# Kernel tuning notes

Measured on AMD Instinct MI355X. Metric: run time of the kernel, lower is better.

The kernel has to match this reference:

```python
import jax, jax.numpy as jnp
import numpy as np

EPS = 1e-6
SLIDING_WINDOW = 512
ROPE_BASE = 10000.0  # rope_local_base_freq for sliding_attention layers


def _rms_norm(x, w=None):
    # Gemma-style RMSNorm computed in fp32 then cast back
    xf = x.astype(jnp.float32)
    out = xf * jax.lax.rsqrt(jnp.mean(xf * xf, axis=-1, keepdims=True) + EPS)
    if w is not None:
        out = out * w.astype(jnp.float32)
    return out.astype(x.dtype)


def _rotate_half(x):
    x1, x2 = jnp.split(x, 2, axis=-1)
    return jnp.concatenate((-x2, x1), axis=-1)


def setup_inputs() -> dict:
    key = jax.random.key(0)
    ks = jax.random.split(key, 6)
    B, S, H, NH, NKV, D = 1, 4096, 2048, 8, 2, 256
    hidden_states = jax.random.normal(ks[0], (B, S, H), dtype=jnp.float32)
    w_q = jax.random.normal(ks[1], (H, NH * D), dtype=jnp.float32) * 0.02
    w_k = jax.random.normal(ks[2], (H, NKV * D), dtype=jnp.float32) * 0.02
    w_v = jax.random.normal(ks[3], (H, NKV * D), dtype=jnp.float32) * 0.02
    w_o = jax.random.normal(ks[4], (NH * D, H), dtype=jnp.float32) * 0.02
    q_norm_w = jnp.ones((D,), dtype=jnp.float32)
    k_norm_w = jnp.ones((D,), dtype=jnp.float32)
    # RoPE tables (local base freq, sliding layer)
    inv_freq = 1.0 / (ROPE_BASE ** (jnp.arange(0, D, 2, dtype=jnp.float32) / D))
    pos = jnp.arange(S, dtype=jnp.float32)
    freqs = pos[:, None] * inv_freq[None, :]          # [S, D/2]
    emb = jnp.concatenate((freqs, freqs), axis=-1)    # [S, D]
    cos = jnp.broadcast_to(jnp.cos(emb)[None], (B, S, D)).astype(jnp.float32)
    sin = jnp.broadcast_to(jnp.sin(emb)[None], (B, S, D)).astype(jnp.float32)
    return {"hidden_states": hidden_states, "w_q": w_q, "w_k": w_k, "w_v": w_v,
            "w_o": w_o, "q_norm_w": q_norm_w, "k_norm_w": k_norm_w,
            "cos": cos, "sin": sin}


def reference(hidden_states, w_q, w_k, w_v, w_o, q_norm_w, k_norm_w, cos, sin):
    B, S, _ = hidden_states.shape
    D = cos.shape[-1]
    NH = w_q.shape[1] // D
    NKV = w_k.shape[1] // D
    G = NH // NKV

    # projections -> [B, S, heads, D], per-head RMSNorm (Gemma3n-style)
    q = _rms_norm((hidden_states @ w_q).reshape(B, S, NH, D), q_norm_w)
    k = _rms_norm((hidden_states @ w_k).reshape(B, S, NKV, D), k_norm_w)
    v = _rms_norm((hidden_states @ w_v).reshape(B, S, NKV, D))  # v_norm: no scale

    q = q.transpose(0, 2, 1, 3)  # [B, NH, S, D]
    k = k.transpose(0, 2, 1, 3)  # [B, NKV, S, D]
    v = v.transpose(0, 2, 1, 3)

    # RoPE, cos/sin unsqueezed over the head dim
    c = cos[:, None, :, :]
    s = sin[:, None, :, :]
    q = q * c + _rotate_half(q) * s
    k = k * c + _rotate_half(k) * s

    # GQA: repeat KV heads
    k = jnp.repeat(k, G, axis=1)  # [B, NH, S, D]
    v = jnp.repeat(v, G, axis=1)

    # attention, scaling = 1.0 (q_norm replaces 1/sqrt(d) in this family)
    scores = jnp.einsum('bhqd,bhkd->bhqk', q, k)

    # causal + sliding-window mask
    i = jnp.arange(S)[:, None]
    j = jnp.arange(S)[None, :]
    mask = (j <= i) & ((i - j) < SLIDING_WINDOW)
    scores = jnp.where(mask[None, None], scores, jnp.finfo(scores.dtype).min)

    attn = jax.nn.softmax(scores.astype(jnp.float32), axis=-1).astype(q.dtype)
    out = jnp.einsum('bhqk,bhkd->bhqd', attn, v)
    out = out.transpose(0, 2, 1, 3).reshape(B, S, NH * D)
    return out @ w_o
```

## Files before the change

### kernel.cpp

```cpp
#include <hip/hip_runtime.h>
#include <hip/hip_bf16.h>

#define S_LEN 4096
#define HDIM  2048
#define NHQ   8
#define NKVH  2
#define DHEAD 256
#define WIN   512
#define NQKV  3072

typedef __hip_bfloat16 bf16_t;
using fragAB = __attribute__((ext_vector_type(8))) short;
using fragC  = __attribute__((ext_vector_type(4))) float;

typedef unsigned int u32;
typedef const __attribute__((address_space(1))) u32* gas_ptr;
typedef __attribute__((address_space(3))) u32* las_ptr;

__device__ __forceinline__ void async_copy16(const void* g, void* l) {
  __builtin_amdgcn_global_load_lds((gas_ptr)g, (las_ptr)l, 16, 0, 0);
}

#define NEG_BIG (-3.0e38f)

__device__ __forceinline__ void split2(float x, bf16_t& hi, bf16_t& lo) {
  bf16_t h = __float2bfloat16(x);
  hi = h;
  lo = __float2bfloat16(x - (float)h);
}

__global__ __launch_bounds__(256) void split_f32(
    const float* __restrict__ in, bf16_t* __restrict__ hi,
    bf16_t* __restrict__ lo, int n) {
  int i = (blockIdx.x * 256 + threadIdx.x) * 4;
  if (i >= n) return;
  float4 v = *(const float4*)(in + i);
  split2(v.x, hi[i + 0], lo[i + 0]);
  split2(v.y, hi[i + 1], lo[i + 1]);
  split2(v.z, hi[i + 2], lo[i + 2]);
  split2(v.w, hi[i + 3], lo[i + 3]);
}

__global__ __launch_bounds__(256) void transpose_cvt(
    const float* __restrict__ in, bf16_t* __restrict__ out, int R, int C) {
  __shared__ bf16_t tile[32][33];
  int c0 = blockIdx.x * 32, r0 = blockIdx.y * 32;
  int tx = threadIdx.x & 31, ty = threadIdx.x >> 5;
#pragma unroll
  for (int i = 0; i < 4; ++i)
    tile[ty + i * 8][tx] = __float2bfloat16(in[(size_t)(r0 + ty + i * 8) * C + c0 + tx]);
  __syncthreads();
#pragma unroll
  for (int i = 0; i < 4; ++i)
    out[(size_t)(c0 + ty + i * 8) * R + r0 + tx] = tile[tx][ty + i * 8];
}

__global__ __launch_bounds__(256) void transpose_split(
    const float* __restrict__ in, bf16_t* __restrict__ hiT,
    bf16_t* __restrict__ loT, int R, int C) {
  __shared__ bf16_t th[32][33];
  __shared__ bf16_t tl[32][33];
  int c0 = blockIdx.x * 32, r0 = blockIdx.y * 32;
  int tx = threadIdx.x & 31, ty = threadIdx.x >> 5;
#pragma unroll
  for (int i = 0; i < 4; ++i) {
    float x = in[(size_t)(r0 + ty + i * 8) * C + c0 + tx];
    bf16_t h, l; split2(x, h, l);
    th[ty + i * 8][tx] = h;
    tl[ty + i * 8][tx] = l;
  }
  __syncthreads();
#pragma unroll
  for (int i = 0; i < 4; ++i) {
    hiT[(size_t)(c0 + ty + i * 8) * R + r0 + tx] = th[tx][ty + i * 8];
    loT[(size_t)(c0 + ty + i * 8) * R + r0 + tx] = tl[tx][ty + i * 8];
  }
}

#define VMCNT_(n) asm volatile("s_waitcnt vmcnt(" #n ")" ::: "memory")
#define VMCNT(n) VMCNT_(n)
#define BARRIER()                     \
  {                                   \
    asm volatile("" ::: "memory");    \
    __builtin_amdgcn_s_barrier();     \
    asm volatile("" ::: "memory");    \
  }

#define MFMA_(a, b, c) __builtin_amdgcn_mfma_f32_16x16x32_bf16(a, b, c, 0, 0, 0)

#define OFF_AH 0
#define OFF_AL 16384
#define OFF_BH 32768
#define OFF_BL 45056
#define BUFSZ  57344

#define LOADB()                                                   \
  _Pragma("unroll")                                               \
  for (int j = 0; j < 3; ++j) {                                   \
    const char* bp_ = bufc + (wn + j * 16 + l16) * 64 + rdq;      \
    bh[j] = *(const fragAB*)(bp_ + OFF_BH);                       \
    bl[j] = *(const fragAB*)(bp_ + OFF_BL);                       \
  }

struct ARegs { fragAB ah0, al0, ah1, al1; };

__device__ __forceinline__ void lda_split(ARegs& r, const char* bufc, int wm,
                                          int p, int l16, int rdq) {
  const char* a0 = bufc + (wm + (2 * p) * 16 + l16) * 64 + rdq;
  const char* a1 = a0 + 16 * 64;
  r.ah0 = *(const fragAB*)(a0 + OFF_AH);
  r.al0 = *(const fragAB*)(a0 + OFF_AL);
  r.ah1 = *(const fragAB*)(a1 + OFF_AH);
  r.al1 = *(const fragAB*)(a1 + OFF_AL);
}

__device__ __forceinline__ void mfma_split(fragC (&acc)[8][3], const ARegs& r,
                                           const fragAB (&bh)[3],
                                           const fragAB (&bl)[3], int p) {
  __builtin_amdgcn_s_setprio(1);
#pragma unroll
  for (int j = 0; j < 3; ++j) {
    acc[2 * p][j]     = MFMA_(r.al0, bh[j], acc[2 * p][j]);
    acc[2 * p + 1][j] = MFMA_(r.al1, bh[j], acc[2 * p + 1][j]);
  }
#pragma unroll
  for (int j = 0; j < 3; ++j) {
    acc[2 * p][j]     = MFMA_(r.ah0, bl[j], acc[2 * p][j]);
    acc[2 * p + 1][j] = MFMA_(r.ah1, bl[j], acc[2 * p + 1][j]);
  }
#pragma unroll
  for (int j = 0; j < 3; ++j) {
    acc[2 * p][j]     = MFMA_(r.ah0, bh[j], acc[2 * p][j]);
    acc[2 * p + 1][j] = MFMA_(r.ah1, bh[j], acc[2 * p + 1][j]);
  }
  __builtin_amdgcn_s_setprio(0);
}

#define SPLIT_STEP()                        \
  {                                         \
    LOADB();                                \
    lda_split(r0, bufc, wm, 0, l16, rdq);   \
    lda_split(r1, bufc, wm, 1, l16, rdq);   \
    mfma_split(acc, r0, bh, bl, 0);         \
    lda_split(r0, bufc, wm, 2, l16, rdq);   \
    mfma_split(acc, r1, bh, bl, 1);         \
    lda_split(r1, bufc, wm, 3, l16, rdq);   \
    mfma_split(acc, r0, bh, bl, 2);         \
    mfma_split(acc, r1, bh, bl, 3);         \
  }

__global__ __launch_bounds__(512, 2) void gemm_split2(
    const bf16_t* __restrict__ Ah, const bf16_t* __restrict__ Al,
    const bf16_t* __restrict__ Bh, const bf16_t* __restrict__ Bl,
    float* __restrict__ C, int M, int N, int K) {
  __shared__ __align__(16) char lds[2 * BUFSZ];
  const int t = threadIdx.x;
  const int wave = t >> 6, lane = t & 63;
  const int quad = lane >> 4, l16 = lane & 15;
  const int m0 = blockIdx.y * 256, n0 = blockIdx.x * 192;
  const int wm = (wave >> 2) * 128, wn = (wave & 3) * 48;
  const int rdq = (quad ^ ((l16 >> 1) & 3)) * 16;

  const size_t laneOff =
      (size_t)(lane >> 2) * K * 2 + 16 * ((lane & 3) ^ ((lane >> 3) & 3));

  const char* gsrc[7];
  int ldsOff[7];
#pragma unroll
  for (int pos = 0; pos < 3; ++pos) {
    int c = wave + 8 * pos;
    if (c < 12) {
      gsrc[pos]   = (const char*)Bh + (size_t)(n0 + 16 * c) * K * 2 + laneOff;
      ldsOff[pos] = OFF_BH + c * 1024;
    } else {
      gsrc[pos]   = (const char*)Bl + (size_t)(n0 + 16 * (c - 12)) * K * 2 + laneOff;
      ldsOff[pos] = OFF_BL + (c - 12) * 1024;
    }
  }
#pragma unroll
  for (int p = 0; p < 4; ++p) {
    int sub = wave & 3;
    int R0 = ((sub >> 1) & 1) * 128 + 32 * p + (sub & 1) * 16;
    const char* base = (const char*)(wave < 4 ? Ah : Al);
    gsrc[3 + p]   = base + (size_t)(m0 + R0) * K * 2 + laneOff;
    ldsOff[3 + p] = (wave < 4 ? OFF_AH : OFF_AL) + R0 * 64;
  }

  fragC zero4 = {0.f, 0.f, 0.f, 0.f};
  fragC acc[8][3];
#pragma unroll
  for (int i = 0; i < 8; ++i)
#pragma unroll
    for (int j = 0; j < 3; ++j) acc[i][j] = zero4;

  char* ldsc = (char*)lds;
#pragma unroll
  for (int ps = 0; ps < 7; ++ps) async_copy16(gsrc[ps], ldsc + ldsOff[ps]);
#pragma unroll
  for (int ps = 0; ps < 7; ++ps) gsrc[ps] += 64;

  fragAB bh[3], bl[3];
  ARegs r0, r1;
  int cur = 0;
  const int NS = K / 32;
  for (int it = 0; it < NS - 1; ++it) {
    const char* bufc = ldsc + cur * BUFSZ;
    char* nb = ldsc + (cur ^ 1) * BUFSZ;
    VMCNT(0); BARRIER();
#pragma unroll
    for (int ps = 0; ps < 7; ++ps) async_copy16(gsrc[ps], nb + ldsOff[ps]);
#pragma unroll
    for (int ps = 0; ps < 7; ++ps) gsrc[ps] += 64;
    SPLIT_STEP();
    cur ^= 1;
  }
  {
    const char* bufc = ldsc + cur * BUFSZ;
    VMCNT(0); BARRIER();
    SPLIT_STEP();
  }

#pragma unroll
  for (int i = 0; i < 8; ++i)
#pragma unroll
    for (int j = 0; j < 3; ++j)
#pragma unroll
      for (int r = 0; r < 4; ++r) {
        int row = m0 + wm + i * 16 + quad * 4 + r;
        int col = n0 + wn + j * 16 + l16;
        C[(size_t)row * N + col] = acc[i][j][r];
      }
}

#define BT_OFF_A 0
#define BT_OFF_B 32768
#define BT_BUFSZ 49152

struct ARegs2 { fragAB a[2][2]; };

__device__ __forceinline__ void lda_bt(ARegs2& r, const char* bufc, int wm,
                                       int p, int l16, int quad, int rx) {
#pragma unroll
  for (int u = 0; u < 2; ++u)
#pragma unroll
    for (int ks = 0; ks < 2; ++ks)
      r.a[u][ks] = *(const fragAB*)(bufc + BT_OFF_A +
                                    (wm + (2 * p + u) * 16 + l16) * 128 +
                                    (((ks * 4 + quad) ^ rx) * 16));
}

__device__ __forceinline__ void mfma_bt(fragC (&acc)[8][2], const ARegs2& r,
                                        const fragAB (&b)[2][2], int p) {
  __builtin_amdgcn_s_setprio(1);
#pragma unroll
  for (int ks = 0; ks < 2; ++ks)
#pragma unroll
    for (int j = 0; j < 2; ++j) {
      acc[2 * p][j]     = MFMA_(r.a[0][ks], b[j][ks], acc[2 * p][j]);
      acc[2 * p + 1][j] = MFMA_(r.a[1][ks], b[j][ks], acc[2 * p + 1][j]);
    }
  __builtin_amdgcn_s_setprio(0);
}

#define BT_LOADB()                                                        \
  _Pragma("unroll")                                                       \
  for (int j = 0; j < 2; ++j)                                             \
  _Pragma("unroll")                                                       \
    for (int ks = 0; ks < 2; ++ks)                                        \
      bfr[j][ks] = *(const fragAB*)(bufc + BT_OFF_B +                     \
                                    (wn + j * 16 + l16) * 128 +           \
                                    (((ks * 4 + quad) ^ rx) * 16));

#define BT_STEP()                                 \
  {                                               \
    BT_LOADB();                                   \
    lda_bt(r0, bufc, wm, 0, l16, quad, rx);       \
    lda_bt(r1, bufc, wm, 1, l16, quad, rx);       \
    mfma_bt(acc, r0, bfr, 0);                     \
    lda_bt(r0, bufc, wm, 2, l16, quad, rx);       \
    mfma_bt(acc, r1, bfr, 1);                     \
    lda_bt(r1, bufc, wm, 3, l16, quad, rx);       \
    mfma_bt(acc, r0, bfr, 2);                     \
    mfma_bt(acc, r1, bfr, 3);                     \
  }

__global__ __launch_bounds__(512, 2) void gemm_bt2(
    const bf16_t* __restrict__ A, const bf16_t* __restrict__ Bt,
    float* __restrict__ C, int M, int N, int K) {
  __shared__ __align__(16) char lds[2 * BT_BUFSZ];
  const int t = threadIdx.x;
  const int wave = t >> 6, lane = t & 63;
  const int quad = lane >> 4, l16 = lane & 15;
  const int m0 = blockIdx.y * 256, n0 = blockIdx.x * 128;
  const int wm = (wave >> 2) * 128, wn = (wave & 3) * 32;
  const int rx = l16 & 7;

  const size_t laneOff =
      (size_t)(lane >> 3) * K * 2 + 16 * ((lane & 7) ^ ((lane >> 3) & 7));

  const char* gsrc[6];
  int ldsOff[6];
#pragma unroll
  for (int pos = 0; pos < 2; ++pos) {
    int c = wave + 8 * pos;
    gsrc[pos]   = (const char*)Bt + (size_t)(n0 + 8 * c) * K * 2 + laneOff;
    ldsOff[pos] = BT_OFF_B + c * 1024;
  }
#pragma unroll
  for (int p = 0; p < 4; ++p) {
    int R0 = (wave >> 2) * 128 + 32 * p + (wave & 3) * 8;
    gsrc[2 + p]   = (const char*)A + (size_t)(m0 + R0) * K * 2 + laneOff;
    ldsOff[2 + p] = BT_OFF_A + R0 * 128;
  }

  fragC zero4 = {0.f, 0.f, 0.f, 0.f};
  fragC acc[8][2];
#pragma unroll
  for (int i = 0; i < 8; ++i)
#pragma unroll
    for (int j = 0; j < 2; ++j) acc[i][j] = zero4;

  char* ldsc = (char*)lds;
#pragma unroll
  for (int ps = 0; ps < 6; ++ps) async_copy16(gsrc[ps], ldsc + ldsOff[ps]);
#pragma unroll
  for (int ps = 0; ps < 6; ++ps) gsrc[ps] += 128;

  fragAB bfr[2][2];
  ARegs2 r0, r1;
  int cur = 0;
  const int NS = K / 64;
  for (int it = 0; it < NS - 1; ++it) {
    const char* bufc = ldsc + cur * BT_BUFSZ;
    char* nb = ldsc + (cur ^ 1) * BT_BUFSZ;
    VMCNT(0); BARRIER();
#pragma unroll
    for (int ps = 0; ps < 6; ++ps) async_copy16(gsrc[ps], nb + ldsOff[ps]);
#pragma unroll
    for (int ps = 0; ps < 6; ++ps) gsrc[ps] += 128;
    BT_STEP();
    cur ^= 1;
  }
  {
    const char* bufc = ldsc + cur * BT_BUFSZ;
    VMCNT(0); BARRIER();
    BT_STEP();
  }

#pragma unroll
  for (int i = 0; i < 8; ++i)
#pragma unroll
    for (int j = 0; j < 2; ++j)
#pragma unroll
      for (int r = 0; r < 4; ++r) {
        int row = m0 + wm + i * 16 + quad * 4 + r;
        int col = n0 + wn + j * 16 + l16;
        C[(size_t)row * N + col] = acc[i][j][r];
      }
}

__global__ __launch_bounds__(256) void rmsnorm_rope_split(
    const float* __restrict__ proj, const float* __restrict__ w,
    const float* __restrict__ cosb, const float* __restrict__ sinb,
    bf16_t* __restrict__ qhi, bf16_t* __restrict__ qlo,
    int inStride, int inOff, int outStride) {
  int s = blockIdx.x, h = blockIdx.y, d = threadIdx.x;
  float x = proj[(size_t)s * inStride + inOff + h * DHEAD + d];
  float ss = x * x;
  ss += __shfl_xor(ss, 1);  ss += __shfl_xor(ss, 2);  ss += __shfl_xor(ss, 4);
  ss += __shfl_xor(ss, 8);  ss += __shfl_xor(ss, 16); ss += __shfl_xor(ss, 32);
  __shared__ float part[4];
  __shared__ float xs[DHEAD];
  if ((threadIdx.x & 63) == 0) part[threadIdx.x >> 6] = ss;
  __syncthreads();
  float tot = part[0] + part[1] + part[2] + part[3];
  float r = rsqrtf(tot * (1.0f / DHEAD) + 1e-6f);
  float xn = x * r * w[d];
  xs[d] = xn;
  __syncthreads();
  float other = xs[(d + 128) & 255];
  float rot = (d < 128) ? -other : other;
  float y = xn * cosb[(size_t)s * DHEAD + d] + rot * sinb[(size_t)s * DHEAD + d];
  bf16_t h2, l2; split2(y, h2, l2);
  size_t oidx = (size_t)s * outStride + h * DHEAD + d;
  qhi[oidx] = h2;
  qlo[oidx] = l2;
}

__global__ __launch_bounds__(256) void rmsnorm_vT(
    const float* __restrict__ proj, bf16_t* __restrict__ vt,
    int inStride, int inOff) {
  int s = blockIdx.x, h = blockIdx.y, d = threadIdx.x;
  float x = proj[(size_t)s * inStride + inOff + h * DHEAD + d];
  float ss = x * x;
  ss += __shfl_xor(ss, 1);  ss += __shfl_xor(ss, 2);  ss += __shfl_xor(ss, 4);
  ss += __shfl_xor(ss, 8);  ss += __shfl_xor(ss, 16); ss += __shfl_xor(ss, 32);
  __shared__ float part[4];
  if ((threadIdx.x & 63) == 0) part[threadIdx.x >> 6] = ss;
  __syncthreads();
  float tot = part[0] + part[1] + part[2] + part[3];
  float r = rsqrtf(tot * (1.0f / DHEAD) + 1e-6f);
  vt[((size_t)h * DHEAD + d) * S_LEN + s] = __float2bfloat16(x * r);
}

__global__ __launch_bounds__(256) void attn_split(
    const bf16_t* __restrict__ Qhi, const bf16_t* __restrict__ Qlo,
    const bf16_t* __restrict__ Khi, const bf16_t* __restrict__ Klo,
    const bf16_t* __restrict__ Vt, bf16_t* __restrict__ Aout) {
  const int h = blockIdx.y;
  const int qb = blockIdx.x * 64;
  const int wave = threadIdx.x >> 6, lane = threadIdx.x & 63;
  const int quad = lane >> 4, l16 = lane & 15;
  const int qw = qb + wave * 16;
  const int kv = h >> 2;
  const bf16_t* Qh_ = Qhi + h * DHEAD;
  const bf16_t* Ql_ = Qlo + h * DHEAD;
  const bf16_t* Kh_ = Khi + kv * DHEAD;
  const bf16_t* Kl_ = Klo + kv * DHEAD;
  const bf16_t* Vh_ = Vt + (size_t)kv * DHEAD * S_LEN;

  __shared__ __align__(16) bf16_t KshH[32 * 256];
  __shared__ __align__(16) bf16_t KshL[32 * 256];
  __shared__ __align__(16) bf16_t Vsh[256 * 32];
  __shared__ __align__(16) bf16_t Plds[4][16 * 32];

  fragAB qfh[8], qfl[8];
#pragma unroll
  for (int c = 0; c < 8; ++c) {
    size_t off = (size_t)(qw + l16) * (NHQ * DHEAD) + c * 32 + quad * 8;
    qfh[c] = *(const fragAB*)(Qh_ + off);
    qfl[c] = *(const fragAB*)(Ql_ + off);
  }

  int kRow[4], kCol[4], vRow[4], vCol[4];
#pragma unroll
  for (int i = 0; i < 4; ++i) {
    int ci = (i * 4 + wave) * 64 + lane;
    int r = ci >> 5, sc = ci & 31;
    kRow[i] = r;
    kCol[i] = (sc ^ r) * 8;
    int rv = ci >> 2, scv = ci & 3;
    vRow[i] = rv;
    vCol[i] = (scv ^ (rv & 3)) * 8;
  }

  fragC zero4 = {0.f, 0.f, 0.f, 0.f};
  fragC o_acc[16];
#pragma unroll
  for (int c = 0; c < 16; ++c) o_acc[c] = zero4;
  float m_run[4] = {NEG_BIG, NEG_BIG, NEG_BIG, NEG_BIG};
  float l_run[4] = {0.f, 0.f, 0.f, 0.f};
  const float LOG2E = 1.4426950408889634f;

  int k_lo = qb - (WIN - 1);
  if (k_lo < 0) k_lo = 0;
  k_lo &= ~31;

  for (int kb = k_lo; kb < qb + 64; kb += 32) {
#pragma unroll
    for (int i = 0; i < 4; ++i) {
      size_t dst = (size_t)(i * 4 + wave) * 1024;
      size_t koff = (size_t)(kb + kRow[i]) * (NKVH * DHEAD) + kCol[i];
      async_copy16(Kh_ + koff, (char*)KshH + dst);
      async_copy16(Kl_ + koff, (char*)KshL + dst);
      async_copy16(Vh_ + (size_t)vRow[i] * S_LEN + kb + vCol[i], (char*)Vsh + dst);
    }
    __syncthreads();

    fragC s0 = zero4, s1 = zero4;
#pragma unroll
    for (int c = 0; c < 8; ++c) {
      int j = c * 4 + quad;
      int off0 = (l16 * 32 + (j ^ l16)) * 16;
      int off1 = ((16 + l16) * 32 + (j ^ (16 + l16))) * 16;
      fragAB kh0 = *(const fragAB*)((const char*)KshH + off0);
      fragAB kl0 = *(const fragAB*)((const char*)KshL + off0);
      fragAB kh1 = *(const fragAB*)((const char*)KshH + off1);
      fragAB kl1 = *(const fragAB*)((const char*)KshL + off1);
      s0 = __builtin_amdgcn_mfma_f32_16x16x32_bf16(qfl[c], kh0, s0, 0, 0, 0);
      s0 = __builtin_amdgcn_mfma_f32_16x16x32_bf16(qfh[c], kl0, s0, 0, 0, 0);
      s0 = __builtin_amdgcn_mfma_f32_16x16x32_bf16(qfh[c], kh0, s0, 0, 0, 0);
      s1 = __builtin_amdgcn_mfma_f32_16x16x32_bf16(qfl[c], kh1, s1, 0, 0, 0);
      s1 = __builtin_amdgcn_mfma_f32_16x16x32_bf16(qfh[c], kl1, s1, 0, 0, 0);
      s1 = __builtin_amdgcn_mfma_f32_16x16x32_bf16(qfh[c], kh1, s1, 0, 0, 0);
    }

    float p0[4], p1[4], alpha[4];
#pragma unroll
    for (int r = 0; r < 4; ++r) {
      int qi = qw + quad * 4 + r;
      int k0i = kb + l16;
      int k1i = k0i + 16;
      bool v0 = (k0i <= qi) && (qi - k0i < WIN);
      bool v1 = (k1i <= qi) && (qi - k1i < WIN);
      float sv0 = v0 ? s0[r] : NEG_BIG;
      float sv1 = v1 ? s1[r] : NEG_BIG;
      float mx = fmaxf(sv0, sv1);
      mx = fmaxf(mx, __shfl_xor(mx, 1));
      mx = fmaxf(mx, __shfl_xor(mx, 2));
      mx = fmaxf(mx, __shfl_xor(mx, 4));
      mx = fmaxf(mx, __shfl_xor(mx, 8));
      float mn = fmaxf(m_run[r], mx);
      float a  = exp2f(fmaxf(m_run[r] - mn, -80.f) * LOG2E);
      float e0 = v0 ? exp2f(fmaxf(s0[r] - mn, -80.f) * LOG2E) : 0.f;
      float e1 = v1 ? exp2f(fmaxf(s1[r] - mn, -80.f) * LOG2E) : 0.f;
      float rs = e0 + e1;
      rs += __shfl_xor(rs, 1);
      rs += __shfl_xor(rs, 2);
      rs += __shfl_xor(rs, 4);
      rs += __shfl_xor(rs, 8);
      l_run[r] = l_run[r] * a + rs;
      m_run[r] = mn;
      alpha[r] = a; p0[r] = e0; p1[r] = e1;
    }
#pragma unroll
    for (int c = 0; c < 16; ++c)
#pragma unroll
      for (int r = 0; r < 4; ++r) o_acc[c][r] *= alpha[r];

    bf16_t* Pw = Plds[wave];
#pragma unroll
    for (int r = 0; r < 4; ++r) {
      Pw[(quad * 4 + r) * 32 + l16]      = __float2bfloat16(p0[r]);
      Pw[(quad * 4 + r) * 32 + 16 + l16] = __float2bfloat16(p1[r]);
    }
    fragAB pf = *(const fragAB*)((const char*)Pw + l16 * 64 + quad * 16);

#pragma unroll
    for (int c = 0; c < 16; ++c) {
      int d = c * 16 + l16;
      int offv = (d * 4 + (quad ^ (d & 3))) * 16;
      fragAB vf = *(const fragAB*)((const char*)Vsh + offv);
      o_acc[c] = __builtin_amdgcn_mfma_f32_16x16x32_bf16(pf, vf, o_acc[c], 0, 0, 0);
    }
    __syncthreads();
  }

  float inv_l[4];
#pragma unroll
  for (int r = 0; r < 4; ++r) inv_l[r] = 1.0f / l_run[r];
#pragma unroll
  for (int c = 0; c < 16; ++c)
#pragma unroll
    for (int r = 0; r < 4; ++r) {
      int row = qw + quad * 4 + r;
      int col = h * DHEAD + c * 16 + l16;
      Aout[(size_t)row * (NHQ * DHEAD) + col] = __float2bfloat16(o_acc[c][r] * inv_l[r]);
    }
}

extern "C" void kernel_launch(void* const* d_in, const int* in_sizes, int n_in,
                              void* d_out, int out_size, void* d_ws, size_t ws_size,
                              hipStream_t stream) {
  const float* hid  = (const float*)d_in[0];
  const float* w_q  = (const float*)d_in[1];
  const float* w_k  = (const float*)d_in[2];
  const float* w_v  = (const float*)d_in[3];
  const float* w_o  = (const float*)d_in[4];
  const float* qnw  = (const float*)d_in[5];
  const float* knw  = (const float*)d_in[6];
  const float* cosb = (const float*)d_in[7];
  const float* sinb = (const float*)d_in[8];
  float* outp = (float*)d_out;

  const size_t M1 = 1048576;
  bf16_t* w = (bf16_t*)d_ws;
  bf16_t* hidh  = w;
  bf16_t* qh    = w;
  bf16_t* hidl  = w + 8 * M1;
  bf16_t* ql    = w + 8 * M1;
  bf16_t* wTh   = w + 16 * M1;
  bf16_t* kh    = w + 16 * M1;
  bf16_t* kl    = w + 18 * M1;
  bf16_t* vt    = w + 20 * M1;
  bf16_t* wTl   = w + 22 * M1;
  bf16_t* woT   = w + 22 * M1;
  float*  projqkv = (float*)(w + 28 * M1);
  bf16_t* aout  = w + 28 * M1;

  split_f32<<<(S_LEN * HDIM) / 1024, 256, 0, stream>>>(hid, hidh, hidl, S_LEN * HDIM);
  transpose_split<<<dim3((NHQ * DHEAD) / 32, HDIM / 32), 256, 0, stream>>>(
      w_q, wTh, wTl, HDIM, NHQ * DHEAD);
  transpose_split<<<dim3((NKVH * DHEAD) / 32, HDIM / 32), 256, 0, stream>>>(
      w_k, wTh + (size_t)(NHQ * DHEAD) * HDIM, wTl + (size_t)(NHQ * DHEAD) * HDIM,
      HDIM, NKVH * DHEAD);
  transpose_split<<<dim3((NKVH * DHEAD) / 32, HDIM / 32), 256, 0, stream>>>(
      w_v, wTh + (size_t)(NHQ * DHEAD + NKVH * DHEAD) * HDIM,
      wTl + (size_t)(NHQ * DHEAD + NKVH * DHEAD) * HDIM, HDIM, NKVH * DHEAD);

  gemm_split2<<<dim3(NQKV / 192, S_LEN / 256), 512, 0, stream>>>(
      hidh, hidl, wTh, wTl, projqkv, S_LEN, NQKV, HDIM);

  rmsnorm_rope_split<<<dim3(S_LEN, NHQ), 256, 0, stream>>>(
      projqkv, qnw, cosb, sinb, qh, ql, NQKV, 0, NHQ * DHEAD);
  rmsnorm_rope_split<<<dim3(S_LEN, NKVH), 256, 0, stream>>>(
      projqkv, knw, cosb, sinb, kh, kl, NQKV, NHQ * DHEAD, NKVH * DHEAD);
  rmsnorm_vT<<<dim3(S_LEN, NKVH), 256, 0, stream>>>(
      projqkv, vt, NQKV, NHQ * DHEAD + NKVH * DHEAD);

  transpose_cvt<<<dim3(HDIM / 32, (NHQ * DHEAD) / 32), 256, 0, stream>>>(w_o, woT, NHQ * DHEAD, HDIM);

  attn_split<<<dim3(S_LEN / 64, NHQ), 256, 0, stream>>>(qh, ql, kh, kl, vt, aout);

  gemm_bt2<<<dim3(HDIM / 128, S_LEN / 256), 512, 0, stream>>>(
      aout, woT, outp, S_LEN, HDIM, NHQ * DHEAD);
}
```

Measured before the change: 440.0 us.

## Enlarge attention tiles to 128 queries and 64-key blocks with 8 waves

The sliding-window attention kernel now uses 512-thread blocks covering 128 query rows and iterates over 64-key blocks instead of 32. Each K/V tile loaded into LDS is shared by twice as many waves, and there are half as many loop iterations and barriers. The LDS swizzle patterns and the P·V MFMA loop are reworked for the wider tiles. The cost is more LDS per block (about 100KB) and fewer blocks in the grid, which may limit occupancy. Coarser 64-aligned key ranges also add some fully masked work at the window edges.

```diff
diff --git a/kernel.cpp b/kernel.cpp
--- a/kernel.cpp
+++ b/kernel.cpp
@@ -403,12 +403,12 @@
   vt[((size_t)h * DHEAD + d) * S_LEN + s] = __float2bfloat16(x * r);
 }
 
-__global__ __launch_bounds__(256) void attn_split(
+__global__ __launch_bounds__(512, 2) void attn_split(
     const bf16_t* __restrict__ Qhi, const bf16_t* __restrict__ Qlo,
     const bf16_t* __restrict__ Khi, const bf16_t* __restrict__ Klo,
     const bf16_t* __restrict__ Vt, bf16_t* __restrict__ Aout) {
   const int h = blockIdx.y;
-  const int qb = blockIdx.x * 64;
+  const int qb = blockIdx.x * 128;
   const int wave = threadIdx.x >> 6, lane = threadIdx.x & 63;
   const int quad = lane >> 4, l16 = lane & 15;
   const int qw = qb + wave * 16;
@@ -419,10 +419,10 @@
   const bf16_t* Kl_ = Klo + kv * DHEAD;
   const bf16_t* Vh_ = Vt + (size_t)kv * DHEAD * S_LEN;
 
-  __shared__ __align__(16) bf16_t KshH[32 * 256];
-  __shared__ __align__(16) bf16_t KshL[32 * 256];
-  __shared__ __align__(16) bf16_t Vsh[256 * 32];
-  __shared__ __align__(16) bf16_t Plds[4][16 * 32];
+  __shared__ __align__(16) bf16_t KshH[64 * 256];
+  __shared__ __align__(16) bf16_t KshL[64 * 256];
+  __shared__ __align__(16) bf16_t Vsh[256 * 64];
+  __shared__ __align__(16) bf16_t Plds[8][16 * 64];
 
   fragAB qfh[8], qfl[8];
 #pragma unroll
@@ -435,13 +435,11 @@
   int kRow[4], kCol[4], vRow[4], vCol[4];
 #pragma unroll
   for (int i = 0; i < 4; ++i) {
-    int ci = (i * 4 + wave) * 64 + lane;
-    int r = ci >> 5, sc = ci & 31;
-    kRow[i] = r;
-    kCol[i] = (sc ^ r) * 8;
-    int rv = ci >> 2, scv = ci & 3;
-    vRow[i] = rv;
-    vCol[i] = (scv ^ (rv & 3)) * 8;
+    int ci = i * 512 + threadIdx.x;
+    kRow[i] = ci >> 5;
+    kCol[i] = ((ci & 31) ^ (kRow[i] & 31)) * 8;
+    vRow[i] = ci >> 3;
+    vCol[i] = ((ci & 7) ^ (vRow[i] & 7)) * 8;
   }
 
   fragC zero4 = {0.f, 0.f, 0.f, 0.f};
@@ -454,12 +452,12 @@
 
   int k_lo = qb - (WIN - 1);
   if (k_lo < 0) k_lo = 0;
-  k_lo &= ~31;
-
-  for (int kb = k_lo; kb < qb + 64; kb += 32) {
+  k_lo &= ~63;
+
+  for (int kb = k_lo; kb < qb + 128; kb += 64) {
 #pragma unroll
     for (int i = 0; i < 4; ++i) {
-      size_t dst = (size_t)(i * 4 + wave) * 1024;
+      size_t dst = (size_t)(i * 512 + threadIdx.x) * 16;
       size_t koff = (size_t)(kb + kRow[i]) * (NKVH * DHEAD) + kCol[i];
       async_copy16(Kh_ + koff, (char*)KshH + dst);
       async_copy16(Kl_ + koff, (char*)KshL + dst);
@@ -467,51 +465,56 @@
     }
     __syncthreads();
 
-    fragC s0 = zero4, s1 = zero4;
+    fragC s[4] = {zero4, zero4, zero4, zero4};
 #pragma unroll
     for (int c = 0; c < 8; ++c) {
       int j = c * 4 + quad;
-      int off0 = (l16 * 32 + (j ^ l16)) * 16;
-      int off1 = ((16 + l16) * 32 + (j ^ (16 + l16))) * 16;
-      fragAB kh0 = *(const fragAB*)((const char*)KshH + off0);
-      fragAB kl0 = *(const fragAB*)((const char*)KshL + off0);
-      fragAB kh1 = *(const fragAB*)((const char*)KshH + off1);
-      fragAB kl1 = *(const fragAB*)((const char*)KshL + off1);
-      s0 = __builtin_amdgcn_mfma_f32_16x16x32_bf16(qfl[c], kh0, s0, 0, 0, 0);
-      s0 = __builtin_amdgcn_mfma_f32_16x16x32_bf16(qfh[c], kl0, s0, 0, 0, 0);
-      s0 = __builtin_amdgcn_mfma_f32_16x16x32_bf16(qfh[c], kh0, s0, 0, 0, 0);
-      s1 = __builtin_amdgcn_mfma_f32_16x16x32_bf16(qfl[c], kh1, s1, 0, 0, 0);
-      s1 = __builtin_amdgcn_mfma_f32_16x16x32_bf16(qfh[c], kl1, s1, 0, 0, 0);
-      s1 = __builtin_amdgcn_mfma_f32_16x16x32_bf16(qfh[c], kh1, s1, 0, 0, 0);
+#pragma unroll
+      for (int g = 0; g < 4; ++g) {
+        int row = g * 16 + l16;
+        int off = (row * 32 + (j ^ (row & 31))) * 16;
+        fragAB kh = *(const fragAB*)((const char*)KshH + off);
+        fragAB kl = *(const fragAB*)((const char*)KshL + off);
+        s[g] = __builtin_amdgcn_mfma_f32_16x16x32_bf16(qfl[c], kh, s[g], 0, 0, 0);
+        s[g] = __builtin_amdgcn_mfma_f32_16x16x32_bf16(qfh[c], kl, s[g], 0, 0, 0);
+        s[g] = __builtin_amdgcn_mfma_f32_16x16x32_bf16(qfh[c], kh, s[g], 0, 0, 0);
+      }
     }
 
-    float p0[4], p1[4], alpha[4];
+    float p[4][4], alpha[4];
 #pragma unroll
     for (int r = 0; r < 4; ++r) {
       int qi = qw + quad * 4 + r;
-      int k0i = kb + l16;
-      int k1i = k0i + 16;
-      bool v0 = (k0i <= qi) && (qi - k0i < WIN);
-      bool v1 = (k1i <= qi) && (qi - k1i < WIN);
-      float sv0 = v0 ? s0[r] : NEG_BIG;
-      float sv1 = v1 ? s1[r] : NEG_BIG;
-      float mx = fmaxf(sv0, sv1);
+      bool vld[4];
+      float sv[4];
+      float mx = NEG_BIG;
+#pragma unroll
+      for (int g = 0; g < 4; ++g) {
+        int ki = kb + g * 16 + l16;
+        vld[g] = (ki <= qi) && (qi - ki < WIN);
+        sv[g] = vld[g] ? s[g][r] : NEG_BIG;
+        mx = fmaxf(mx, sv[g]);
+      }
       mx = fmaxf(mx, __shfl_xor(mx, 1));
       mx = fmaxf(mx, __shfl_xor(mx, 2));
       mx = fmaxf(mx, __shfl_xor(mx, 4));
       mx = fmaxf(mx, __shfl_xor(mx, 8));
       float mn = fmaxf(m_run[r], mx);
       float a  = exp2f(fmaxf(m_run[r] - mn, -80.f) * LOG2E);
-      float e0 = v0 ? exp2f(fmaxf(s0[r] - mn, -80.f) * LOG2E) : 0.f;
-      float e1 = v1 ? exp2f(fmaxf(s1[r] - mn, -80.f) * LOG2E) : 0.f;
-      float rs = e0 + e1;
+      float rs = 0.f;
+#pragma unroll
+      for (int g = 0; g < 4; ++g) {
+        float e = vld[g] ? exp2f(fmaxf(s[g][r] - mn, -80.f) * LOG2E) : 0.f;
+        p[g][r] = e;
+        rs += e;
+      }
       rs += __shfl_xor(rs, 1);
       rs += __shfl_xor(rs, 2);
       rs += __shfl_xor(rs, 4);
       rs += __shfl_xor(rs, 8);
       l_run[r] = l_run[r] * a + rs;
       m_run[r] = mn;
-      alpha[r] = a; p0[r] = e0; p1[r] = e1;
+      alpha[r] = a;
     }
 #pragma unroll
     for (int c = 0; c < 16; ++c)
@@ -520,18 +523,23 @@
 
     bf16_t* Pw = Plds[wave];
 #pragma unroll
-    for (int r = 0; r < 4; ++r) {
-      Pw[(quad * 4 + r) * 32 + l16]      = __float2bfloat16(p0[r]);
-      Pw[(quad * 4 + r) * 32 + 16 + l16] = __float2bfloat16(p1[r]);
-    }
-    fragAB pf = *(const fragAB*)((const char*)Pw + l16 * 64 + quad * 16);
+    for (int r = 0; r < 4; ++r)
+#pragma unroll
+      for (int g = 0; g < 4; ++g)
+        Pw[(quad * 4 + r) * 64 + g * 16 + l16] = __float2bfloat16(p[g][r]);
+    fragAB pf0 = *(const fragAB*)((const char*)Pw + l16 * 128 + quad * 16);
+    fragAB pf1 = *(const fragAB*)((const char*)Pw + l16 * 128 + 64 + quad * 16);
 
 #pragma unroll
     for (int c = 0; c < 16; ++c) {
       int d = c * 16 + l16;
-      int offv = (d * 4 + (quad ^ (d & 3))) * 16;
-      fragAB vf = *(const fragAB*)((const char*)Vsh + offv);
-      o_acc[c] = __builtin_amdgcn_mfma_f32_16x16x32_bf16(pf, vf, o_acc[c], 0, 0, 0);
+#pragma unroll
+      for (int ks = 0; ks < 2; ++ks) {
+        int offv = (d * 8 + ((ks * 4 + quad) ^ (d & 7))) * 16;
+        fragAB vf = *(const fragAB*)((const char*)Vsh + offv);
+        o_acc[c] = __builtin_amdgcn_mfma_f32_16x16x32_bf16(
+            ks == 0 ? pf0 : pf1, vf, o_acc[c], 0, 0, 0);
+      }
     }
     __syncthreads();
   }
@@ -600,7 +608,7 @@
 
   transpose_cvt<<<dim3(HDIM / 32, (NHQ * DHEAD) / 32), 256, 0, stream>>>(w_o, woT, NHQ * DHEAD, HDIM);
 
-  attn_split<<<dim3(S_LEN / 64, NHQ), 256, 0, stream>>>(qh, ql, kh, kl, vt, aout);
+  attn_split<<<dim3(S_LEN / 128, NHQ), 512, 0, stream>>>(qh, ql, kh, kl, vt, aout);
 
   gemm_bt2<<<dim3(HDIM / 128, S_LEN / 256), 512, 0, stream>>>(
       aout, woT, outp, S_LEN, HDIM, NHQ * DHEAD);
```

Measured after the change: 419.4 us. 1.05x faster.
